# Optimization experiments

Hardware: AMD Instinct MI355X
Metric: run time of the kernel (lower is better)

Reference implementation:

```python
import jax, jax.numpy as jnp
import numpy as np

N_NODES = 50000
N_EDGES = 800000
N_FEAT = 128
N_HIDDEN = 128
N_CLASSES = 64


def sage_mean_conv(x, src, dst, W_self, W_neigh, b, n_nodes):
    # DGL SAGEConv (mean): out = x @ W_self + mean_neigh(x) @ W_neigh + b
    # mean over in-neighbors: messages flow src -> dst
    msg = x[src]  # [E, F] gather
    h_sum = jax.ops.segment_sum(msg, dst, num_segments=n_nodes)  # [N, F]
    deg = jax.ops.segment_sum(jnp.ones((src.shape[0],), x.dtype), dst,
                              num_segments=n_nodes)
    h_mean = h_sum / jnp.maximum(deg, 1.0)[:, None]
    return x @ W_self + h_mean @ W_neigh + b


def setup_inputs() -> dict:
    key = jax.random.key(0)
    ks = jax.random.split(key, 8)
    sc1 = 1.0 / np.sqrt(N_FEAT)
    sc2 = 1.0 / np.sqrt(N_HIDDEN)
    return {
        "x": jax.random.normal(ks[0], (N_NODES, N_FEAT), jnp.float32),
        "W_self1": jax.random.normal(ks[1], (N_FEAT, N_HIDDEN), jnp.float32) * sc1,
        "W_neigh1": jax.random.normal(ks[2], (N_FEAT, N_HIDDEN), jnp.float32) * sc1,
        "b1": jnp.zeros((N_HIDDEN,), jnp.float32),
        "W_self2": jax.random.normal(ks[3], (N_HIDDEN, N_CLASSES), jnp.float32) * sc2,
        "W_neigh2": jax.random.normal(ks[4], (N_HIDDEN, N_CLASSES), jnp.float32) * sc2,
        "b2": jnp.zeros((N_CLASSES,), jnp.float32),
        "src": jax.random.randint(ks[5], (N_EDGES,), 0, N_NODES, jnp.int32),
        "dst": jax.random.randint(ks[6], (N_EDGES,), 0, N_NODES, jnp.int32),
    }


def reference(x, W_self1, W_neigh1, b1, W_self2, W_neigh2, b2, src, dst):
    n = x.shape[0]
    h = sage_mean_conv(x, src, dst, W_self1, W_neigh1, b1, n)
    h = jax.nn.relu(h)
    logits = sage_mean_conv(h, src, dst, W_self2, W_neigh2, b2, n)
    return logits
```

## Files before the change

### kernel.cpp

```cpp
#include <hip/hip_runtime.h>
#include <hip/hip_fp16.h>

#define N_NODES 50000
#define N_EDGES 800000
#define N_FEAT 128
#define N_HIDDEN 128
#define N_CLASSES 64

#define NBUCK 256
#define BUCK_NODES 196
#define BIN_CHUNK 2048
#define BIN_BLK ((N_EDGES + BIN_CHUNK - 1) / BIN_CHUNK)

#define PACK1_BLK 16
#define PACK2_BLK 8
#define PREP_BLK (BIN_BLK + PACK1_BLK + PACK2_BLK)
#define GEMM1_BLK ((N_NODES + 31) / 32)
#define BG_BLK (BIN_BLK + GEMM1_BLK)

typedef __attribute__((ext_vector_type(8))) short bf16x8;
typedef __attribute__((ext_vector_type(4))) float f32x4;
typedef __attribute__((ext_vector_type(2))) float f32x2;

__device__ __forceinline__ unsigned short f32_to_bf16(float f) {
    unsigned int u = __float_as_uint(f);
    return (unsigned short)((u + 0x7fffu + ((u >> 16) & 1u)) >> 16);
}
__device__ __forceinline__ float bf16lo(unsigned int v) { return __uint_as_float(v << 16); }
__device__ __forceinline__ float bf16hi(unsigned int v) { return __uint_as_float(v & 0xffff0000u); }

#if defined(__has_builtin)
#if __has_builtin(__builtin_amdgcn_cvt_pk_f32_fp8) && __has_builtin(__builtin_amdgcn_cvt_pk_fp8_f32)
#define FP8_HW 1
#endif
#endif

__device__ __forceinline__ unsigned char f32_to_fp8(float f) {
#ifdef FP8_HW
    return (unsigned char)(__builtin_amdgcn_cvt_pk_fp8_f32(f, f, 0, false) & 0xff);
#else
    unsigned short hb = __half_as_ushort(__float2half(f));
    return (unsigned char)((hb + 0x7fu + ((hb >> 8) & 1u)) >> 8);
#endif
}

__device__ __forceinline__ void fp8x4_to_f32(unsigned int u, float* o) {
#ifdef FP8_HW
    f32x2 lo = __builtin_amdgcn_cvt_pk_f32_fp8(u, false);
    f32x2 hi = __builtin_amdgcn_cvt_pk_f32_fp8(u, true);
    o[0] = lo.x; o[1] = lo.y; o[2] = hi.x; o[3] = hi.y;
#else
    o[0] = __half2float(__ushort_as_half((unsigned short)((u & 0xffu) << 8)));
    o[1] = __half2float(__ushort_as_half((unsigned short)(((u >> 8) & 0xffu) << 8)));
    o[2] = __half2float(__ushort_as_half((unsigned short)(((u >> 16) & 0xffu) << 8)));
    o[3] = __half2float(__ushort_as_half((unsigned short)(((u >> 24) & 0xffu) << 8)));
#endif
}

template <int NOUT>
__device__ void pack_w_body(int idx, const float* __restrict__ Wself,
                            const float* __restrict__ Wneigh,
                            unsigned short* __restrict__ Bp) {
    constexpr int NT = NOUT / 16;
    constexpr int NO = NOUT / 2;
    if (idx >= 4 * NT * 64) return;
    const int lane = idx & 63;
    const int tc = idx >> 6;
    const int c = tc % NT;
    const int t = tc / NT;
    const int n = c * 16 + (lane & 15);
    const int k0 = t * 32 + (lane >> 4) * 8;
    const float* W = (n < NO) ? Wself : Wneigh;
    const int nn = (n < NO) ? n : n - NO;
    ushort4 lo, hi;
    lo.x = f32_to_bf16(W[(k0 + 0) * NO + nn]);
    lo.y = f32_to_bf16(W[(k0 + 1) * NO + nn]);
    lo.z = f32_to_bf16(W[(k0 + 2) * NO + nn]);
    lo.w = f32_to_bf16(W[(k0 + 3) * NO + nn]);
    hi.x = f32_to_bf16(W[(k0 + 4) * NO + nn]);
    hi.y = f32_to_bf16(W[(k0 + 5) * NO + nn]);
    hi.z = f32_to_bf16(W[(k0 + 6) * NO + nn]);
    hi.w = f32_to_bf16(W[(k0 + 7) * NO + nn]);
    ((ushort4*)&Bp[(size_t)idx * 8])[0] = lo;
    ((ushort4*)&Bp[(size_t)idx * 8])[1] = hi;
}

__device__ void a0_body(int blk, const int* __restrict__ dst, int* __restrict__ hists) {
    __shared__ int h[NBUCK];
    const int t = threadIdx.x;
    h[t] = 0;
    __syncthreads();
    const int lo = blk * BIN_CHUNK;
    const int hi = min(lo + BIN_CHUNK, N_EDGES);
    for (int i = lo + t; i < hi; i += 256) {
        atomicAdd(&h[dst[i] / BUCK_NODES], 1);
    }
    __syncthreads();
    hists[blk * NBUCK + t] = h[t];
}

__global__ __launch_bounds__(256) void prep_kernel(
        const int* __restrict__ dst, int* __restrict__ hists,
        const float* __restrict__ Ws1, const float* __restrict__ Wn1,
        unsigned short* __restrict__ Bp1,
        const float* __restrict__ Ws2, const float* __restrict__ Wn2,
        unsigned short* __restrict__ Bp2) {
    const int b = blockIdx.x;
    const int t = threadIdx.x;
    if (b < BIN_BLK) {
        a0_body(b, dst, hists);
    } else if (b < BIN_BLK + PACK1_BLK) {
        int idx = (b - BIN_BLK) * 256 + t;
        pack_w_body<256>(idx, Ws1, Wn1, Bp1);
    } else {
        int idx = (b - BIN_BLK - PACK1_BLK) * 256 + t;
        pack_w_body<128>(idx, Ws2, Wn2, Bp2);
    }
}

__global__ __launch_bounds__(256) void bscan_kernel(const int* __restrict__ hists,
                                                    int* __restrict__ bstart,
                                                    int* __restrict__ bcursor) {
    __shared__ int sc[NBUCK];
    const int t = threadIdx.x;
    int v = 0;
#pragma unroll 8
    for (int c = 0; c < BIN_BLK; ++c) v += hists[c * NBUCK + t];
    sc[t] = v;
    __syncthreads();
    for (int s = 1; s < NBUCK; s <<= 1) {
        int u = (t >= s) ? sc[t - s] : 0;
        __syncthreads();
        sc[t] += u;
        __syncthreads();
    }
    const int excl = sc[t] - v;
    bstart[t] = excl;
    bcursor[t] = excl;
    if (t == NBUCK - 1) bstart[NBUCK] = sc[t];
}

__device__ void a1_body(int blk, const int* __restrict__ src, const int* __restrict__ dst,
                        const int* __restrict__ hists,
                        int* __restrict__ bcursor, unsigned int* __restrict__ binned) {
    __shared__ int base[NBUCK];
    __shared__ int cnt[NBUCK];
    const int t = threadIdx.x;
    const int h = hists[blk * NBUCK + t];
    base[t] = atomicAdd(&bcursor[t], h);
    cnt[t] = 0;
    __syncthreads();
    const int lo = blk * BIN_CHUNK;
    const int hi = min(lo + BIN_CHUNK, N_EDGES);
    for (int i = lo + t; i < hi; i += 256) {
        const int d = dst[i];
        const int b = d / BUCK_NODES;
        const int r = atomicAdd(&cnt[b], 1);
        binned[base[b] + r] = ((unsigned int)(d - b * BUCK_NODES) << 16) | (unsigned int)src[i];
    }
}

__device__ __forceinline__ bf16x8 load_a_f32(const float* base) {
    float4 u = ((const float4*)base)[0];
    float4 v = ((const float4*)base)[1];
    bf16x8 a;
    a[0] = (short)f32_to_bf16(u.x); a[1] = (short)f32_to_bf16(u.y);
    a[2] = (short)f32_to_bf16(u.z); a[3] = (short)f32_to_bf16(u.w);
    a[4] = (short)f32_to_bf16(v.x); a[5] = (short)f32_to_bf16(v.y);
    a[6] = (short)f32_to_bf16(v.z); a[7] = (short)f32_to_bf16(v.w);
    return a;
}

template <int NOUT, bool AF32, bool SB16, bool PFP8>
__device__ void gemm_mfma_body(int gblk,
                               const float* __restrict__ af,
                               const unsigned short* __restrict__ ab,
                               const unsigned short* __restrict__ Bp,
                               const float* __restrict__ bias,
                               float* __restrict__ s32,
                               unsigned short* __restrict__ s16,
                               unsigned char* __restrict__ p8,
                               unsigned short* __restrict__ p16) {
    constexpr int NT = NOUT / 16;
    constexpr int NO = NOUT / 2;
    constexpr int NSUB = NT / 4;

    const int tid = threadIdx.x;
    const int wave = tid >> 6;
    const int lane = tid & 63;
    const int mcol = lane & 15;
    const int kgrp = lane >> 4;

    const int mbase = gblk * 32;
    int r0 = mbase + mcol;       if (r0 >= N_NODES) r0 = N_NODES - 1;
    int r1 = mbase + 16 + mcol;  if (r1 >= N_NODES) r1 = N_NODES - 1;

    f32x4 acc[2][NSUB];
#pragma unroll
    for (int mt = 0; mt < 2; ++mt)
#pragma unroll
        for (int c = 0; c < NSUB; ++c)
            acc[mt][c] = (f32x4){0.f, 0.f, 0.f, 0.f};

#pragma unroll
    for (int t = 0; t < 4; ++t) {
        bf16x8 a0, a1;
        if (AF32) {
            a0 = load_a_f32(&af[(size_t)r0 * 128 + t * 32 + kgrp * 8]);
            a1 = load_a_f32(&af[(size_t)r1 * 128 + t * 32 + kgrp * 8]);
        } else {
            a0 = *(const bf16x8*)&ab[(size_t)r0 * 128 + t * 32 + kgrp * 8];
            a1 = *(const bf16x8*)&ab[(size_t)r1 * 128 + t * 32 + kgrp * 8];
        }
#pragma unroll
        for (int c = 0; c < NSUB; ++c) {
            const int ct = wave * NSUB + c;
            bf16x8 bfrag = *(const bf16x8*)&Bp[((size_t)(t * NT + ct) * 64 + lane) * 8];
            acc[0][c] = __builtin_amdgcn_mfma_f32_16x16x32_bf16(a0, bfrag, acc[0][c], 0, 0, 0);
            acc[1][c] = __builtin_amdgcn_mfma_f32_16x16x32_bf16(a1, bfrag, acc[1][c], 0, 0, 0);
        }
    }

    float bv[NSUB];
    int ncols[NSUB];
#pragma unroll
    for (int c = 0; c < NSUB; ++c) {
        ncols[c] = (wave * NSUB + c) * 16 + mcol;
        bv[c] = (ncols[c] < NO) ? bias[ncols[c]] : 0.f;
    }

#pragma unroll
    for (int mt = 0; mt < 2; ++mt) {
#pragma unroll
        for (int c = 0; c < NSUB; ++c) {
            const int ncol = ncols[c];
#pragma unroll
            for (int r = 0; r < 4; ++r) {
                const int node = mbase + mt * 16 + kgrp * 4 + r;
                if (node >= N_NODES) continue;
                const float v = acc[mt][c][r];
                if (ncol < NO) {
                    if (SB16) s16[(size_t)node * NO + ncol] = f32_to_bf16(v + bv[c]);
                    else      s32[(size_t)node * NO + ncol] = v + bv[c];
                } else if (PFP8) {
                    p8[(size_t)node * NO + (ncol - NO)] = f32_to_fp8(v);
                } else {
                    p16[(size_t)node * NO + (ncol - NO)] = f32_to_bf16(v);
                }
            }
        }
    }
}

__global__ __launch_bounds__(256) void bin_gemm1_kernel(
        const int* __restrict__ src, const int* __restrict__ dst,
        const int* __restrict__ hists,
        int* __restrict__ bcursor, unsigned int* __restrict__ binned,
        const float* __restrict__ x,
        const unsigned short* __restrict__ Bp1,
        const float* __restrict__ b1,
        unsigned short* __restrict__ s1, unsigned char* __restrict__ p1) {
    const int b = blockIdx.x;
    if (b < BIN_BLK) {
        a1_body(b, src, dst, hists, bcursor, binned);
    } else {
        gemm_mfma_body<256, true, true, true>(b - BIN_BLK, x, nullptr, Bp1, b1,
                                              nullptr, s1, p1, nullptr);
    }
}

__global__ __launch_bounds__(256) void bucket_build_kernel(
        const unsigned int* __restrict__ binned,
        const int* __restrict__ bstart,
        int* __restrict__ offsets,
        unsigned short* __restrict__ csr16) {
    __shared__ int cnt[NBUCK];
    __shared__ int pre[NBUCK];
    const int b = blockIdx.x;
    const int t = threadIdx.x;
    const int n0 = b * BUCK_NODES;
    const int nn = min(N_NODES - n0, BUCK_NODES);
    const int e0 = bstart[b];
    const int e1 = bstart[b + 1];

    cnt[t] = 0;
    __syncthreads();
    for (int i = e0 + t; i < e1; i += 256) {
        atomicAdd(&cnt[binned[i] >> 16], 1);
    }
    __syncthreads();
    int v = cnt[t];
    pre[t] = v;
    __syncthreads();
    for (int s = 1; s < NBUCK; s <<= 1) {
        int u = (t >= s) ? pre[t - s] : 0;
        __syncthreads();
        pre[t] += u;
        __syncthreads();
    }
    const int excl = pre[t] - v;
    if (t < nn) offsets[n0 + t] = e0 + excl;
    if (b == 0 && t == 0) offsets[N_NODES] = N_EDGES;
    __syncthreads();
    pre[t] = excl;
    cnt[t] = 0;
    __syncthreads();
    for (int i = e0 + t; i < e1; i += 256) {
        const unsigned int u = binned[i];
        const int dl = (int)(u >> 16);
        const int r = atomicAdd(&cnt[dl], 1);
        csr16[e0 + pre[dl] + r] = (unsigned short)(u & 0xffffu);
    }
}

__global__ __launch_bounds__(256) void gemm2_kernel(
        const unsigned short* __restrict__ h1b,
        const unsigned short* __restrict__ Bp2,
        const float* __restrict__ b2,
        float* __restrict__ s2, unsigned short* __restrict__ p2) {
    gemm_mfma_body<128, false, false, false>(blockIdx.x, nullptr, h1b, Bp2, b2,
                                             s2, nullptr, nullptr, p2);
}

__global__ __launch_bounds__(256) void agg_relu_128_kernel(
        const unsigned short* __restrict__ s16,
        const unsigned char* __restrict__ p,
        const int* __restrict__ offsets,
        const unsigned short* __restrict__ csr16,
        unsigned short* __restrict__ h1b) {
    const int wave = threadIdx.x >> 6;
    const int lane = threadIdx.x & 63;
    const int q = lane >> 4;
    const int l = lane & 15;
    const int node = blockIdx.x * 4 + wave;
    if (node >= N_NODES) return;

    const int off0 = offsets[node];
    const int off1 = offsets[node + 1];
    const uint2* pp = (const uint2*)p;

    float a[8];
#pragma unroll
    for (int k = 0; k < 8; ++k) a[k] = 0.f;

    for (int i = off0 + q; i < off1; i += 32) {
        int idx[8];
        float m[8];
        uint2 w[8];
#pragma unroll
        for (int j = 0; j < 8; ++j) {
            const int e = i + 4 * j;
            const int ec = min(e, off1 - 1);
            idx[j] = (int)csr16[ec];
            m[j] = (e < off1) ? 1.f : 0.f;
        }
#pragma unroll
        for (int j = 0; j < 8; ++j) w[j] = pp[(size_t)idx[j] * 16 + l];
#pragma unroll
        for (int j = 0; j < 8; ++j) {
            float d0[4], d1[4];
            fp8x4_to_f32(w[j].x, d0);
            fp8x4_to_f32(w[j].y, d1);
            a[0] += m[j] * d0[0]; a[1] += m[j] * d0[1];
            a[2] += m[j] * d0[2]; a[3] += m[j] * d0[3];
            a[4] += m[j] * d1[0]; a[5] += m[j] * d1[1];
            a[6] += m[j] * d1[2]; a[7] += m[j] * d1[3];
        }
    }
#pragma unroll
    for (int k = 0; k < 8; ++k) {
        a[k] += __shfl_xor(a[k], 16);
        a[k] += __shfl_xor(a[k], 32);
    }

    if (q == 0) {
        const float invdeg = 1.0f / fmaxf((float)(off1 - off0), 1.0f);
        uint4 sw = ((const uint4*)s16)[(size_t)node * 16 + l];
        float sf[8];
        sf[0] = bf16lo(sw.x); sf[1] = bf16hi(sw.x);
        sf[2] = bf16lo(sw.y); sf[3] = bf16hi(sw.y);
        sf[4] = bf16lo(sw.z); sf[5] = bf16hi(sw.z);
        sf[6] = bf16lo(sw.w); sf[7] = bf16hi(sw.w);
        ushort4 o0, o1;
        o0.x = f32_to_bf16(fmaxf(sf[0] + a[0] * invdeg, 0.f));
        o0.y = f32_to_bf16(fmaxf(sf[1] + a[1] * invdeg, 0.f));
        o0.z = f32_to_bf16(fmaxf(sf[2] + a[2] * invdeg, 0.f));
        o0.w = f32_to_bf16(fmaxf(sf[3] + a[3] * invdeg, 0.f));
        o1.x = f32_to_bf16(fmaxf(sf[4] + a[4] * invdeg, 0.f));
        o1.y = f32_to_bf16(fmaxf(sf[5] + a[5] * invdeg, 0.f));
        o1.z = f32_to_bf16(fmaxf(sf[6] + a[6] * invdeg, 0.f));
        o1.w = f32_to_bf16(fmaxf(sf[7] + a[7] * invdeg, 0.f));
        ((ushort4*)h1b)[(size_t)node * 32 + l * 2] = o0;
        ((ushort4*)h1b)[(size_t)node * 32 + l * 2 + 1] = o1;
    }
}

__global__ __launch_bounds__(256) void agg_64_kernel(
        const unsigned short* __restrict__ p,
        const int* __restrict__ offsets,
        const unsigned short* __restrict__ csr16,
        float* __restrict__ out) {
    const int wave = threadIdx.x >> 6;
    const int lane = threadIdx.x & 63;
    const int st = lane >> 3;
    const int l = lane & 7;
    const int node = blockIdx.x * 4 + wave;
    if (node >= N_NODES) return;

    const int off0 = offsets[node];
    const int off1 = offsets[node + 1];
    const uint4* pp = (const uint4*)p;

    float a[8];
#pragma unroll
    for (int k = 0; k < 8; ++k) a[k] = 0.f;

    for (int i = off0 + st; i < off1; i += 32) {
        int idx[4];
        float m[4];
        uint4 w[4];
#pragma unroll
        for (int j = 0; j < 4; ++j) {
            const int e = i + 8 * j;
            const int ec = min(e, off1 - 1);
            idx[j] = (int)csr16[ec];
            m[j] = (e < off1) ? 1.f : 0.f;
        }
#pragma unroll
        for (int j = 0; j < 4; ++j) w[j] = pp[(size_t)idx[j] * 8 + l];
#pragma unroll
        for (int j = 0; j < 4; ++j) {
            a[0] += m[j] * bf16lo(w[j].x); a[1] += m[j] * bf16hi(w[j].x);
            a[2] += m[j] * bf16lo(w[j].y); a[3] += m[j] * bf16hi(w[j].y);
            a[4] += m[j] * bf16lo(w[j].z); a[5] += m[j] * bf16hi(w[j].z);
            a[6] += m[j] * bf16lo(w[j].w); a[7] += m[j] * bf16hi(w[j].w);
        }
    }
#pragma unroll
    for (int k = 0; k < 8; ++k) {
        a[k] += __shfl_xor(a[k], 8);
        a[k] += __shfl_xor(a[k], 16);
        a[k] += __shfl_xor(a[k], 32);
    }

    if (st == 0) {
        const float invdeg = 1.0f / fmaxf((float)(off1 - off0), 1.0f);
        float4 s0 = ((float4*)out)[(size_t)node * 16 + l * 2];
        float4 s1 = ((float4*)out)[(size_t)node * 16 + l * 2 + 1];
        s0.x += a[0] * invdeg; s0.y += a[1] * invdeg;
        s0.z += a[2] * invdeg; s0.w += a[3] * invdeg;
        s1.x += a[4] * invdeg; s1.y += a[5] * invdeg;
        s1.z += a[6] * invdeg; s1.w += a[7] * invdeg;
        ((float4*)out)[(size_t)node * 16 + l * 2] = s0;
        ((float4*)out)[(size_t)node * 16 + l * 2 + 1] = s1;
    }
}

extern "C" void kernel_launch(void* const* d_in, const int* in_sizes, int n_in,
                              void* d_out, int out_size, void* d_ws, size_t ws_size,
                              hipStream_t stream) {
    const float* x        = (const float*)d_in[0];
    const float* W_self1  = (const float*)d_in[1];
    const float* W_neigh1 = (const float*)d_in[2];
    const float* b1       = (const float*)d_in[3];
    const float* W_self2  = (const float*)d_in[4];
    const float* W_neigh2 = (const float*)d_in[5];
    const float* b2       = (const float*)d_in[6];
    const int*   src      = (const int*)d_in[7];
    const int*   dst      = (const int*)d_in[8];
    float* out = (float*)d_out;

    int* bstart  = (int*)d_ws;
    int* bcursor = bstart + 288;
    int* offsets = bcursor + 256;
    int* hists   = offsets + 50048;
    unsigned int* binned = (unsigned int*)(hists + BIN_BLK * NBUCK);
    unsigned short* csr16 = (unsigned short*)(binned + 800000);
    unsigned short* Bp1 = csr16 + 800000;
    unsigned short* Bp2 = Bp1 + 32768;
    unsigned short* s1  = Bp2 + 16384;
    unsigned short* h1b = s1 + (size_t)N_NODES * 128;
    unsigned char* p1   = (unsigned char*)(h1b + (size_t)N_NODES * 128);
    unsigned short* p2  = (unsigned short*)p1;

    prep_kernel<<<PREP_BLK, 256, 0, stream>>>(dst, hists,
                                              W_self1, W_neigh1, Bp1,
                                              W_self2, W_neigh2, Bp2);
    bscan_kernel<<<1, 256, 0, stream>>>(hists, bstart, bcursor);
    bin_gemm1_kernel<<<BG_BLK, 256, 0, stream>>>(src, dst, hists, bcursor, binned,
                                                 x, Bp1, b1, s1, p1);
    bucket_build_kernel<<<NBUCK, 256, 0, stream>>>(binned, bstart, offsets, csr16);
    agg_relu_128_kernel<<<(N_NODES + 3) / 4, 256, 0, stream>>>(s1, p1, offsets, csr16, h1b);
    gemm2_kernel<<<(N_NODES + 31) / 32, 256, 0, stream>>>(h1b, Bp2, b2, out, p2);
    agg_64_kernel<<<(N_NODES + 3) / 4, 256, 0, stream>>>(p2, offsets, csr16, out);
}
```

Measured before the change: 208.0 us.

## Double bucket count, parallelize histogram column sums, vectorize edge binning loads

Raises the bucket count from 256 to 512 with half as many nodes per bucket, so bucket_build runs across more blocks with smaller local scans. The serial single-block column reduction over all bin histograms becomes a separate multi-block colsum kernel with wavefront shuffles, followed by a small scan kernel. The histogram and binning loops now read dst/src as int4 vectors. This adds one extra kernel launch and doubles the histogram memory and global cursor atomics. The int4 loop relies on chunk boundaries being multiples of 4, which holds here.

```diff
diff --git a/kernel.cpp b/kernel.cpp
--- a/kernel.cpp
+++ b/kernel.cpp
@@ -7,8 +7,8 @@
 #define N_HIDDEN 128
 #define N_CLASSES 64
 
-#define NBUCK 256
-#define BUCK_NODES 196
+#define NBUCK 512
+#define BUCK_NODES 98
 #define BIN_CHUNK 2048
 #define BIN_BLK ((N_EDGES + BIN_CHUNK - 1) / BIN_CHUNK)
 
@@ -89,14 +89,20 @@
     __shared__ int h[NBUCK];
     const int t = threadIdx.x;
     h[t] = 0;
+    h[t + 256] = 0;
     __syncthreads();
     const int lo = blk * BIN_CHUNK;
     const int hi = min(lo + BIN_CHUNK, N_EDGES);
-    for (int i = lo + t; i < hi; i += 256) {
-        atomicAdd(&h[dst[i] / BUCK_NODES], 1);
+    for (int i4 = (lo >> 2) + t; i4 < (hi >> 2); i4 += 256) {
+        int4 d = ((const int4*)dst)[i4];
+        atomicAdd(&h[d.x / BUCK_NODES], 1);
+        atomicAdd(&h[d.y / BUCK_NODES], 1);
+        atomicAdd(&h[d.z / BUCK_NODES], 1);
+        atomicAdd(&h[d.w / BUCK_NODES], 1);
     }
     __syncthreads();
     hists[blk * NBUCK + t] = h[t];
+    hists[blk * NBUCK + t + 256] = h[t + 256];
 }
 
 __global__ __launch_bounds__(256) void prep_kernel(
@@ -118,14 +124,23 @@
     }
 }
 
-__global__ __launch_bounds__(256) void bscan_kernel(const int* __restrict__ hists,
+__global__ __launch_bounds__(64) void colsum_kernel(const int* __restrict__ hists,
+                                                    int* __restrict__ colsum) {
+    const int b = blockIdx.x;
+    const int t = threadIdx.x;
+    int v = 0;
+    for (int c = t; c < BIN_BLK; c += 64) v += hists[c * NBUCK + b];
+#pragma unroll
+    for (int s = 32; s > 0; s >>= 1) v += __shfl_down(v, s);
+    if (t == 0) colsum[b] = v;
+}
+
+__global__ __launch_bounds__(512) void bscan_kernel(const int* __restrict__ colsum,
                                                     int* __restrict__ bstart,
                                                     int* __restrict__ bcursor) {
     __shared__ int sc[NBUCK];
     const int t = threadIdx.x;
-    int v = 0;
-#pragma unroll 8
-    for (int c = 0; c < BIN_BLK; ++c) v += hists[c * NBUCK + t];
+    const int v = colsum[t];
     sc[t] = v;
     __syncthreads();
     for (int s = 1; s < NBUCK; s <<= 1) {
@@ -146,17 +161,28 @@
     __shared__ int base[NBUCK];
     __shared__ int cnt[NBUCK];
     const int t = threadIdx.x;
-    const int h = hists[blk * NBUCK + t];
-    base[t] = atomicAdd(&bcursor[t], h);
-    cnt[t] = 0;
+    {
+        const int h0 = hists[blk * NBUCK + t];
+        const int h1 = hists[blk * NBUCK + t + 256];
+        base[t] = atomicAdd(&bcursor[t], h0);
+        base[t + 256] = atomicAdd(&bcursor[t + 256], h1);
+        cnt[t] = 0;
+        cnt[t + 256] = 0;
+    }
     __syncthreads();
     const int lo = blk * BIN_CHUNK;
     const int hi = min(lo + BIN_CHUNK, N_EDGES);
-    for (int i = lo + t; i < hi; i += 256) {
-        const int d = dst[i];
-        const int b = d / BUCK_NODES;
-        const int r = atomicAdd(&cnt[b], 1);
-        binned[base[b] + r] = ((unsigned int)(d - b * BUCK_NODES) << 16) | (unsigned int)src[i];
+    for (int i4 = (lo >> 2) + t; i4 < (hi >> 2); i4 += 256) {
+        int4 d = ((const int4*)dst)[i4];
+        int4 s = ((const int4*)src)[i4];
+#pragma unroll
+        for (int j = 0; j < 4; ++j) {
+            const int dj = (j == 0) ? d.x : (j == 1) ? d.y : (j == 2) ? d.z : d.w;
+            const int sj = (j == 0) ? s.x : (j == 1) ? s.y : (j == 2) ? s.z : s.w;
+            const int b = dj / BUCK_NODES;
+            const int r = atomicAdd(&cnt[b], 1);
+            binned[base[b] + r] = ((unsigned int)(dj - b * BUCK_NODES) << 16) | (unsigned int)sj;
+        }
     }
 }
 
@@ -274,8 +300,8 @@
         const int* __restrict__ bstart,
         int* __restrict__ offsets,
         unsigned short* __restrict__ csr16) {
-    __shared__ int cnt[NBUCK];
-    __shared__ int pre[NBUCK];
+    __shared__ int cnt[128];
+    __shared__ int pre[128];
     const int b = blockIdx.x;
     const int t = threadIdx.x;
     const int n0 = b * BUCK_NODES;
@@ -283,27 +309,29 @@
     const int e0 = bstart[b];
     const int e1 = bstart[b + 1];
 
-    cnt[t] = 0;
+    if (t < 128) cnt[t] = 0;
     __syncthreads();
     for (int i = e0 + t; i < e1; i += 256) {
         atomicAdd(&cnt[binned[i] >> 16], 1);
     }
     __syncthreads();
-    int v = cnt[t];
-    pre[t] = v;
-    __syncthreads();
-    for (int s = 1; s < NBUCK; s <<= 1) {
-        int u = (t >= s) ? pre[t - s] : 0;
+    if (t < 128) {
+        pre[t] = cnt[t];
+    }
+    __syncthreads();
+    for (int s = 1; s < 128; s <<= 1) {
+        int u = (t < 128 && t >= s) ? pre[t - s] : 0;
         __syncthreads();
-        pre[t] += u;
+        if (t < 128) pre[t] += u;
         __syncthreads();
     }
-    const int excl = pre[t] - v;
-    if (t < nn) offsets[n0 + t] = e0 + excl;
+    if (t < 128) {
+        const int excl = pre[t] - cnt[t];
+        if (t < nn) offsets[n0 + t] = e0 + excl;
+        pre[t] = excl;
+        cnt[t] = 0;
+    }
     if (b == 0 && t == 0) offsets[N_NODES] = N_EDGES;
-    __syncthreads();
-    pre[t] = excl;
-    cnt[t] = 0;
     __syncthreads();
     for (int i = e0 + t; i < e1; i += 256) {
         const unsigned int u = binned[i];
@@ -471,8 +499,9 @@
     float* out = (float*)d_out;
 
     int* bstart  = (int*)d_ws;
-    int* bcursor = bstart + 288;
-    int* offsets = bcursor + 256;
+    int* bcursor = bstart + 544;
+    int* colsum  = bcursor + 512;
+    int* offsets = colsum + 512;
     int* hists   = offsets + 50048;
     unsigned int* binned = (unsigned int*)(hists + BIN_BLK * NBUCK);
     unsigned short* csr16 = (unsigned short*)(binned + 800000);
@@ -486,7 +515,8 @@
     prep_kernel<<<PREP_BLK, 256, 0, stream>>>(dst, hists,
                                               W_self1, W_neigh1, Bp1,
                                               W_self2, W_neigh2, Bp2);
-    bscan_kernel<<<1, 256, 0, stream>>>(hists, bstart, bcursor);
+    colsum_kernel<<<NBUCK, 64, 0, stream>>>(hists, colsum);
+    bscan_kernel<<<1, NBUCK, 0, stream>>>(colsum, bstart, bcursor);
     bin_gemm1_kernel<<<BG_BLK, 256, 0, stream>>>(src, dst, hists, bcursor, binned,
                                                  x, Bp1, b1, s1, p1);
     bucket_build_kernel<<<NBUCK, 256, 0, stream>>>(binned, bstart, offsets, csr16);
```

Result: faster. 196.7 us, median of 2 (-5.5%).
